# Kernel tuning notes

Measured on AMD Instinct MI355X. Metric: run time of the kernel, lower is better.

Reference implementation:

```python
import jax, jax.numpy as jnp
import numpy as np

N_NODES = 10000
N_EDGES = 160000
DIM_IN = 32
DIM_OUT = 64
DIM_EDGE_HIDDEN = 128
BOND_FDIM = 13


def setup_inputs() -> dict:
    key = jax.random.key(0)
    ks = jax.random.split(key, 10)
    s = 0.1
    x = jax.random.normal(ks[0], (N_NODES, DIM_IN), dtype=jnp.float32)
    edge_index = jax.random.randint(ks[1], (2, N_EDGES), 0, N_NODES, dtype=jnp.int64)
    edge_attr = jax.random.uniform(ks[2], (N_EDGES, BOND_FDIM), dtype=jnp.float32)
    # edge-MLP params: BOND_FDIM -> hidden -> in*out
    W1 = jax.random.normal(ks[3], (BOND_FDIM, DIM_EDGE_HIDDEN), dtype=jnp.float32) * s
    b1 = jnp.zeros((DIM_EDGE_HIDDEN,), dtype=jnp.float32)
    W2 = jax.random.normal(ks[4], (DIM_EDGE_HIDDEN, DIM_IN * DIM_OUT), dtype=jnp.float32) * s
    b2 = jnp.zeros((DIM_IN * DIM_OUT,), dtype=jnp.float32)
    # NNConv root weight + bias
    root = jax.random.normal(ks[5], (DIM_IN, DIM_OUT), dtype=jnp.float32) * s
    bias = jnp.zeros((DIM_OUT,), dtype=jnp.float32)
    return {"x": x, "edge_index": edge_index, "edge_attr": edge_attr,
            "W1": W1, "b1": b1, "W2": W2, "b2": b2, "root": root, "bias": bias}


def reference(x, edge_index, edge_attr, W1, b1, W2, b2, root, bias):
    src, dst = edge_index[0], edge_index[1]  # PyG: row=source j, col=target i
    # edge MLP -> per-edge weight matrix [E, in, out]
    h = jax.nn.relu(edge_attr @ W1 + b1)
    w = (h @ W2 + b2).reshape(-1, DIM_IN, DIM_OUT)
    # gather source features, per-edge matmul -> messages [E, out]
    msg = jnp.einsum('ei,eio->eo', x[src], w)
    # scatter-add to target nodes
    agg = jax.ops.segment_sum(msg, dst, num_segments=N_NODES)
    out = agg + x @ root + bias
    return jax.nn.relu(out)
```

## Files before the change

kernel.cpp:

```cpp
#include <hip/hip_runtime.h>

#define N_NODES 10000
#define N_EDGES 160000
#define DIM_IN 32
#define DIM_OUT 64
#define DIM_HID 128
#define BOND 13
#define NB 4
#define NGROUPS (N_NODES / NB)
#define CAP 96

typedef _Float16 half2_t __attribute__((ext_vector_type(2)));
typedef _Float16 f16x8 __attribute__((ext_vector_type(8)));
typedef float f32x4 __attribute__((ext_vector_type(4)));
typedef unsigned int uint;
typedef unsigned short ushort;

static __device__ __forceinline__ float fdot2u(uint a, uint b, float c) {
#if __has_builtin(__builtin_amdgcn_fdot2)
    return __builtin_amdgcn_fdot2(__builtin_bit_cast(half2_t, a),
                                  __builtin_bit_cast(half2_t, b), c, false);
#else
    half2_t ha = __builtin_bit_cast(half2_t, a);
    half2_t hb = __builtin_bit_cast(half2_t, b);
    return c + (float)ha.x * (float)hb.x + (float)ha.y * (float)hb.y;
#endif
}

static __device__ __forceinline__ uint packh2(float a, float b) {
    half2_t h;
    h.x = (_Float16)a; h.y = (_Float16)b;
    return __builtin_bit_cast(uint, h);
}

static __device__ __forceinline__ int swz(int o, int kp) { return (o + kp) & 63; }

struct EScr {
    int      eids[64];
    int      dsts[64];
    _Float16 ea16[16][32];
    _Float16 hbuf16[16][136];
};

__global__ void prep_kernel(const float* __restrict__ W2, uint* __restrict__ W2p,
                            const float* __restrict__ W1, uint4* __restrict__ W1p,
                            const int* __restrict__ ei, int* __restrict__ cnt,
                            int* __restrict__ es,
                            const float* __restrict__ x, const float* __restrict__ root,
                            const float* __restrict__ bias, float* __restrict__ out) {
    int idx = blockIdx.x * 256 + threadIdx.x;
    if (idx < 16 * 64 * DIM_HID) {
        int ip = idx >> 13;
        int o  = (idx >> 7) & 63;
        int k  = idx & 127;
        float lo = W2[k * 2048 + (2 * ip) * 64 + o];
        float hi = W2[k * 2048 + (2 * ip + 1) * 64 + o];
        W2p[idx] = packh2(lo, hi);
    }
    if (idx < 512) {
        int nh = idx >> 6, lane = idx & 63;
        int quad = lane >> 4, l15 = lane & 15;
        int col = nh * 16 + l15;
        uint u[4];
#pragma unroll
        for (int jp = 0; jp < 4; ++jp) {
            int k0 = quad * 8 + 2 * jp, k1 = k0 + 1;
            float f0 = (k0 < BOND) ? W1[k0 * DIM_HID + col] : 0.f;
            float f1 = (k1 < BOND) ? W1[k1 * DIM_HID + col] : 0.f;
            u[jp] = packh2(f0, f1);
        }
        W1p[idx] = make_uint4(u[0], u[1], u[2], u[3]);
    }
    if (idx < N_NODES * DIM_OUT) {
        int n = idx >> 6, o = idx & 63;
        float r = bias[o];
        const float* xn = x + n * DIM_IN;
#pragma unroll 8
        for (int i = 0; i < DIM_IN; ++i) r += xn[i] * root[i * DIM_OUT + o];
        out[idx] = r;
    }
    if (idx < N_EDGES) {
        int src = ei[idx];
        int slot = atomicAdd(&cnt[src], 1);
        if (slot < CAP) es[src * CAP + slot] = idx;
    }
}

__global__ __launch_bounds__(256) void phase1_kernel(
    const float* __restrict__ x, const int* __restrict__ ei,
    const float* __restrict__ ea, const uint4* __restrict__ W1p,
    const float* __restrict__ b1, const uint* __restrict__ W2p,
    const float* __restrict__ b2, const int* __restrict__ cnt,
    const int* __restrict__ es, float* __restrict__ out)
{
    __shared__ uint  Ph[NB][DIM_HID / 2][DIM_OUT];
    __shared__ float xs_t[DIM_IN][NB];
    __shared__ uint  xsp[DIM_IN / 2][NB];

    const int t  = threadIdx.x;
    const int o  = t & 63;
    const int w  = t >> 6;
    const int n0 = blockIdx.x * NB;
    const int l15  = o & 15;
    const int quad = o >> 4;

    if (t < DIM_IN * NB) {
        int i = t >> 2, j = t & 3;
        xs_t[i][j] = x[(n0 + j) * DIM_IN + i];
    }
    __syncthreads();
    if (t < (DIM_IN / 2) * NB) {
        int ip = t >> 2, j = t & 3;
        xsp[ip][j] = packh2(xs_t[2 * ip][j], xs_t[2 * ip + 1][j]);
    }
    __syncthreads();

#pragma unroll 1
    for (int ot = 0; ot < 4; ++ot) {
        float acc[2][NB][4];
#pragma unroll
        for (int l = 0; l < 2; ++l)
#pragma unroll
            for (int j = 0; j < NB; ++j)
#pragma unroll
                for (int q = 0; q < 4; ++q) acc[l][j][q] = 0.f;
#pragma unroll 4
        for (int ip = 0; ip < 16; ++ip) {
            const uint4* base4 = (const uint4*)W2p + ((ip * 64 + ot * 16) << 5);
            uint4 wv0 = base4[w * 128 + o];
            uint4 wv1 = base4[w * 128 + 64 + o];
            uint xp0 = xsp[ip][0], xp1 = xsp[ip][1];
            uint xp2 = xsp[ip][2], xp3 = xsp[ip][3];
#define ACC4(l, wv, xp, j) \
            acc[l][j][0] = fdot2u(xp, wv.x, acc[l][j][0]); \
            acc[l][j][1] = fdot2u(xp, wv.y, acc[l][j][1]); \
            acc[l][j][2] = fdot2u(xp, wv.z, acc[l][j][2]); \
            acc[l][j][3] = fdot2u(xp, wv.w, acc[l][j][3]);
            ACC4(0, wv0, xp0, 0) ACC4(0, wv0, xp1, 1)
            ACC4(0, wv0, xp2, 2) ACC4(0, wv0, xp3, 3)
            ACC4(1, wv1, xp0, 0) ACC4(1, wv1, xp1, 1)
            ACC4(1, wv1, xp2, 2) ACC4(1, wv1, xp3, 3)
#undef ACC4
        }
        const int lhi = o >> 5;
        const int kq  = o & 31;
        const int o0 = ot * 16 + w * 4 + lhi;
        const int o1 = o0 + 2;
        const int kp0 = 2 * kq, kp1 = 2 * kq + 1;
#pragma unroll
        for (int j = 0; j < NB; ++j) {
            Ph[j][kp0][swz(o0, kp0)] = packh2(acc[0][j][0], acc[0][j][1]);
            Ph[j][kp1][swz(o0, kp1)] = packh2(acc[0][j][2], acc[0][j][3]);
            Ph[j][kp0][swz(o1, kp0)] = packh2(acc[1][j][0], acc[1][j][1]);
            Ph[j][kp1][swz(o1, kp1)] = packh2(acc[1][j][2], acc[1][j][3]);
        }
    }
    __syncthreads();

    f16x8 pregf[16];
#pragma unroll
    for (int nt = 0; nt < 4; ++nt)
#pragma unroll
        for (int kk = 0; kk < 4; ++kk) {
            const int col = nt * 16 + l15;
            uint4 u;
            int kp = kk * 16 + quad * 4;
            u.x = Ph[w][kp + 0][swz(col, kp + 0)];
            u.y = Ph[w][kp + 1][swz(col, kp + 1)];
            u.z = Ph[w][kp + 2][swz(col, kp + 2)];
            u.w = Ph[w][kp + 3][swz(col, kp + 3)];
            pregf[nt * 4 + kk] = __builtin_bit_cast(f16x8, u);
        }

    float qv[4] = {0.f, 0.f, 0.f, 0.f};
#pragma unroll 4
    for (int i = 0; i < DIM_IN; ++i) {
        float xv = xs_t[i][w];
#pragma unroll
        for (int nt = 0; nt < 4; ++nt)
            qv[nt] += xv * b2[i * DIM_OUT + nt * 16 + l15];
    }

    f16x8 w1f[8];
    float b1v[8];
#pragma unroll
    for (int nh = 0; nh < 8; ++nh) {
        w1f[nh] = __builtin_bit_cast(f16x8, W1p[nh * 64 + o]);
        b1v[nh] = b1[nh * 16 + l15];
    }

    EScr* S = (EScr*)&Ph[w][0][0];
    const int n = n0 + w;
    const int start = n * CAP;
    int deg = cnt[n];
    deg = deg < CAP ? deg : CAP;

    __builtin_amdgcn_wave_barrier();
    ((uint4*)S->ea16)[o] = make_uint4(0u, 0u, 0u, 0u);
    __builtin_amdgcn_wave_barrier();

#pragma unroll 1
    for (int gbase = 0; gbase < deg; gbase += 64) {
        const int cnt64 = (deg - gbase < 64) ? (deg - gbase) : 64;
        __builtin_amdgcn_wave_barrier();
        if (o < cnt64) {
            int e = es[start + gbase + o];
            S->eids[o] = e;
            S->dsts[o] = ei[N_EDGES + e];
        }
        __builtin_amdgcn_wave_barrier();
        const int ntiles = (cnt64 + 15) >> 4;
#pragma unroll 1
        for (int tb = 0; tb < ntiles; ++tb) {
            const int tilebase = tb * 16;
            const int tcnt = (cnt64 - tilebase < 16) ? (cnt64 - tilebase) : 16;
            __builtin_amdgcn_wave_barrier();
            if (l15 < BOND) {
#pragma unroll
                for (int r = 0; r < 4; ++r) {
                    int p = quad + 4 * r;
                    if (p < tcnt) {
                        float v = ea[(long)S->eids[tilebase + p] * BOND + l15];
                        S->ea16[p][l15] = (_Float16)v;
                    }
                }
            }
            __builtin_amdgcn_wave_barrier();
            const f16x8 af = *(const f16x8*)&S->ea16[l15][quad * 8];
#pragma unroll
            for (int nh = 0; nh < 8; ++nh) {
                f32x4 hacc = {0.f, 0.f, 0.f, 0.f};
                hacc = __builtin_amdgcn_mfma_f32_16x16x32_f16(af, w1f[nh], hacc, 0, 0, 0);
#pragma unroll
                for (int r = 0; r < 4; ++r) {
                    float hv = hacc[r] + b1v[nh];
                    S->hbuf16[quad * 4 + r][nh * 16 + l15] =
                        (_Float16)(hv > 0.f ? hv : 0.f);
                }
            }
            __builtin_amdgcn_wave_barrier();
            f16x8 hf[4];
#pragma unroll
            for (int kk = 0; kk < 4; ++kk)
                hf[kk] = *(const f16x8*)&S->hbuf16[l15][kk * 32 + quad * 8];
            int dstv[4];
#pragma unroll
            for (int r = 0; r < 4; ++r)
                dstv[r] = S->dsts[tilebase + quad * 4 + r];
#pragma unroll
            for (int nt = 0; nt < 4; ++nt) {
                f32x4 acc = {0.f, 0.f, 0.f, 0.f};
#pragma unroll
                for (int kk = 0; kk < 4; ++kk)
                    acc = __builtin_amdgcn_mfma_f32_16x16x32_f16(
                              hf[kk], pregf[nt * 4 + kk], acc, 0, 0, 0);
#pragma unroll
                for (int r = 0; r < 4; ++r) {
                    if (quad * 4 + r < tcnt)
                        atomicAdd(&out[(long)dstv[r] * DIM_OUT + nt * 16 + l15],
                                  acc[r] + qv[nt]);
                }
            }
        }
    }
}

__global__ __launch_bounds__(256) void relu_kernel(float* __restrict__ out) {
    int idx = blockIdx.x * 256 + threadIdx.x;
    if (idx < N_NODES * DIM_OUT) {
        float v = out[idx];
        out[idx] = v > 0.f ? v : 0.f;
    }
}


extern "C" void kernel_launch(void* const* d_in, const int* in_sizes, int n_in,
                              void* d_out, int out_size, void* d_ws, size_t ws_size,
                              hipStream_t stream) {
    const float* x    = (const float*)d_in[0];
    const int*   ei   = (const int*)d_in[1];
    const float* ea   = (const float*)d_in[2];
    const float* W1   = (const float*)d_in[3];
    const float* b1   = (const float*)d_in[4];
    const float* W2   = (const float*)d_in[5];
    const float* b2   = (const float*)d_in[6];
    const float* root = (const float*)d_in[7];
    const float* bias = (const float*)d_in[8];
    float* out = (float*)d_out;
    char* ws = (char*)d_ws;

    int*   cnt = (int*)(ws + 0);
    int*   es  = (int*)(ws + 40064);
    uint*  W2p = (uint*)(ws + 3880064);
    uint4* W1p = (uint4*)(ws + 4404352);

    hipMemsetAsync(cnt, 0, 40064, stream);
    prep_kernel<<<2500, 256, 0, stream>>>(W2, W2p, W1, W1p, ei, cnt, es,
                                          x, root, bias, out);
    phase1_kernel<<<NGROUPS, 256, 0, stream>>>(x, ei, ea, W1p, b1, W2p, b2,
                                               cnt, es, out);
    relu_kernel<<<2500, 256, 0, stream>>>(out);
}
```

Baseline: 199.1 us.

## Compute per-node projected W2 with MFMA and split node edges across two waves

```diff
diff --git a/kernel.cpp b/kernel.cpp
--- a/kernel.cpp
+++ b/kernel.cpp
@@ -6,7 +6,7 @@
 #define DIM_OUT 64
 #define DIM_HID 128
 #define BOND 13
-#define NB 4
+#define NB 8
 #define NGROUPS (N_NODES / NB)
 #define CAP 96
 
@@ -14,18 +14,6 @@
 typedef _Float16 f16x8 __attribute__((ext_vector_type(8)));
 typedef float f32x4 __attribute__((ext_vector_type(4)));
 typedef unsigned int uint;
-typedef unsigned short ushort;
-
-static __device__ __forceinline__ float fdot2u(uint a, uint b, float c) {
-#if __has_builtin(__builtin_amdgcn_fdot2)
-    return __builtin_amdgcn_fdot2(__builtin_bit_cast(half2_t, a),
-                                  __builtin_bit_cast(half2_t, b), c, false);
-#else
-    half2_t ha = __builtin_bit_cast(half2_t, a);
-    half2_t hb = __builtin_bit_cast(half2_t, b);
-    return c + (float)ha.x * (float)hb.x + (float)ha.y * (float)hb.y;
-#endif
-}
 
 static __device__ __forceinline__ uint packh2(float a, float b) {
     half2_t h;
@@ -36,26 +24,29 @@
 static __device__ __forceinline__ int swz(int o, int kp) { return (o + kp) & 63; }
 
 struct EScr {
-    int      eids[64];
-    int      dsts[64];
+    int      eids[16];
+    int      dsts[16];
     _Float16 ea16[16][32];
     _Float16 hbuf16[16][136];
 };
 
-__global__ void prep_kernel(const float* __restrict__ W2, uint* __restrict__ W2p,
+__global__ void prep_kernel(const float* __restrict__ W2, uint4* __restrict__ W2p,
                             const float* __restrict__ W1, uint4* __restrict__ W1p,
                             const int* __restrict__ ei, int* __restrict__ cnt,
                             int* __restrict__ es,
                             const float* __restrict__ x, const float* __restrict__ root,
                             const float* __restrict__ bias, float* __restrict__ out) {
     int idx = blockIdx.x * 256 + threadIdx.x;
-    if (idx < 16 * 64 * DIM_HID) {
-        int ip = idx >> 13;
-        int o  = (idx >> 7) & 63;
-        int k  = idx & 127;
-        float lo = W2[k * 2048 + (2 * ip) * 64 + o];
-        float hi = W2[k * 2048 + (2 * ip + 1) * 64 + o];
-        W2p[idx] = packh2(lo, hi);
+    if (idx < 512 * 64) {
+        int f = idx >> 6, lane = idx & 63;
+        int k = f >> 2, of = f & 3;
+        int q = lane >> 4, l15 = lane & 15;
+        const float* base = W2 + k * 2048 + q * 512 + of * 16 + l15;
+        uint u0 = packh2(base[0],   base[64]);
+        uint u1 = packh2(base[128], base[192]);
+        uint u2 = packh2(base[256], base[320]);
+        uint u3 = packh2(base[384], base[448]);
+        W2p[idx] = make_uint4(u0, u1, u2, u3);
     }
     if (idx < 512) {
         int nh = idx >> 6, lane = idx & 63;
@@ -86,16 +77,14 @@
     }
 }
 
-__global__ __launch_bounds__(256) void phase1_kernel(
+__global__ __launch_bounds__(1024, 4) void phase1_kernel(
     const float* __restrict__ x, const int* __restrict__ ei,
     const float* __restrict__ ea, const uint4* __restrict__ W1p,
-    const float* __restrict__ b1, const uint* __restrict__ W2p,
+    const float* __restrict__ b1, const uint4* __restrict__ W2p,
     const float* __restrict__ b2, const int* __restrict__ cnt,
     const int* __restrict__ es, float* __restrict__ out)
 {
     __shared__ uint  Ph[NB][DIM_HID / 2][DIM_OUT];
-    __shared__ float xs_t[DIM_IN][NB];
-    __shared__ uint  xsp[DIM_IN / 2][NB];
 
     const int t  = threadIdx.x;
     const int o  = t & 63;
@@ -104,59 +93,50 @@
     const int l15  = o & 15;
     const int quad = o >> 4;
 
-    if (t < DIM_IN * NB) {
-        int i = t >> 2, j = t & 3;
-        xs_t[i][j] = x[(n0 + j) * DIM_IN + i];
+    f16x8 af;
+    {
+        uint ua[4];
+        const float* xn8 = x + (long)(n0 + l15) * DIM_IN;
+#pragma unroll
+        for (int jj = 0; jj < 4; ++jj) {
+            float a0 = 0.f, a1 = 0.f;
+            if (l15 < NB) {
+                a0 = xn8[quad * 8 + 2 * jj];
+                a1 = xn8[quad * 8 + 2 * jj + 1];
+            }
+            ua[jj] = packh2(a0, a1);
+        }
+        af = __builtin_bit_cast(f16x8, make_uint4(ua[0], ua[1], ua[2], ua[3]));
+    }
+
+    {
+        const int of = w & 3;
+        const int kbase = (w >> 2) * 32;
+        const int oo = of * 16 + l15;
+#pragma unroll 2
+        for (int m = 0; m < 16; ++m) {
+            const int k0 = kbase + 2 * m;
+            const uint4 bu0 = W2p[(k0 * 4 + of) * 64 + o];
+            const uint4 bu1 = W2p[((k0 + 1) * 4 + of) * 64 + o];
+            f32x4 D0 = {0.f, 0.f, 0.f, 0.f};
+            f32x4 D1 = {0.f, 0.f, 0.f, 0.f};
+            D0 = __builtin_amdgcn_mfma_f32_16x16x32_f16(
+                     af, __builtin_bit_cast(f16x8, bu0), D0, 0, 0, 0);
+            D1 = __builtin_amdgcn_mfma_f32_16x16x32_f16(
+                     af, __builtin_bit_cast(f16x8, bu1), D1, 0, 0, 0);
+            if (o < 32) {
+                const int kp = (kbase >> 1) + m;
+                const int sc = swz(oo, kp);
+#pragma unroll
+                for (int r = 0; r < 4; ++r)
+                    Ph[quad * 4 + r][kp][sc] = packh2(D0[r], D1[r]);
+            }
+        }
     }
     __syncthreads();
-    if (t < (DIM_IN / 2) * NB) {
-        int ip = t >> 2, j = t & 3;
-        xsp[ip][j] = packh2(xs_t[2 * ip][j], xs_t[2 * ip + 1][j]);
-    }
-    __syncthreads();
-
-#pragma unroll 1
-    for (int ot = 0; ot < 4; ++ot) {
-        float acc[2][NB][4];
-#pragma unroll
-        for (int l = 0; l < 2; ++l)
-#pragma unroll
-            for (int j = 0; j < NB; ++j)
-#pragma unroll
-                for (int q = 0; q < 4; ++q) acc[l][j][q] = 0.f;
-#pragma unroll 4
-        for (int ip = 0; ip < 16; ++ip) {
-            const uint4* base4 = (const uint4*)W2p + ((ip * 64 + ot * 16) << 5);
-            uint4 wv0 = base4[w * 128 + o];
-            uint4 wv1 = base4[w * 128 + 64 + o];
-            uint xp0 = xsp[ip][0], xp1 = xsp[ip][1];
-            uint xp2 = xsp[ip][2], xp3 = xsp[ip][3];
-#define ACC4(l, wv, xp, j) \
-            acc[l][j][0] = fdot2u(xp, wv.x, acc[l][j][0]); \
-            acc[l][j][1] = fdot2u(xp, wv.y, acc[l][j][1]); \
-            acc[l][j][2] = fdot2u(xp, wv.z, acc[l][j][2]); \
-            acc[l][j][3] = fdot2u(xp, wv.w, acc[l][j][3]);
-            ACC4(0, wv0, xp0, 0) ACC4(0, wv0, xp1, 1)
-            ACC4(0, wv0, xp2, 2) ACC4(0, wv0, xp3, 3)
-            ACC4(1, wv1, xp0, 0) ACC4(1, wv1, xp1, 1)
-            ACC4(1, wv1, xp2, 2) ACC4(1, wv1, xp3, 3)
-#undef ACC4
-        }
-        const int lhi = o >> 5;
-        const int kq  = o & 31;
-        const int o0 = ot * 16 + w * 4 + lhi;
-        const int o1 = o0 + 2;
-        const int kp0 = 2 * kq, kp1 = 2 * kq + 1;
-#pragma unroll
-        for (int j = 0; j < NB; ++j) {
-            Ph[j][kp0][swz(o0, kp0)] = packh2(acc[0][j][0], acc[0][j][1]);
-            Ph[j][kp1][swz(o0, kp1)] = packh2(acc[0][j][2], acc[0][j][3]);
-            Ph[j][kp0][swz(o1, kp0)] = packh2(acc[1][j][0], acc[1][j][1]);
-            Ph[j][kp1][swz(o1, kp1)] = packh2(acc[1][j][2], acc[1][j][3]);
-        }
-    }
-    __syncthreads();
-
+
+    const int nd  = w >> 1;
+    const int sub = w & 1;
     f16x8 pregf[16];
 #pragma unroll
     for (int nt = 0; nt < 4; ++nt)
@@ -165,20 +145,25 @@
             const int col = nt * 16 + l15;
             uint4 u;
             int kp = kk * 16 + quad * 4;
-            u.x = Ph[w][kp + 0][swz(col, kp + 0)];
-            u.y = Ph[w][kp + 1][swz(col, kp + 1)];
-            u.z = Ph[w][kp + 2][swz(col, kp + 2)];
-            u.w = Ph[w][kp + 3][swz(col, kp + 3)];
+            u.x = Ph[nd][kp + 0][swz(col, kp + 0)];
+            u.y = Ph[nd][kp + 1][swz(col, kp + 1)];
+            u.z = Ph[nd][kp + 2][swz(col, kp + 2)];
+            u.w = Ph[nd][kp + 3][swz(col, kp + 3)];
             pregf[nt * 4 + kk] = __builtin_bit_cast(f16x8, u);
         }
 
+    const int n = n0 + nd;
+
     float qv[4] = {0.f, 0.f, 0.f, 0.f};
+    {
+        const float* xn = x + (long)n * DIM_IN;
 #pragma unroll 4
-    for (int i = 0; i < DIM_IN; ++i) {
-        float xv = xs_t[i][w];
-#pragma unroll
-        for (int nt = 0; nt < 4; ++nt)
-            qv[nt] += xv * b2[i * DIM_OUT + nt * 16 + l15];
+        for (int i = 0; i < DIM_IN; ++i) {
+            float xv = xn[i];
+#pragma unroll
+            for (int nt = 0; nt < 4; ++nt)
+                qv[nt] += xv * b2[i * DIM_OUT + nt * 16 + l15];
+        }
     }
 
     f16x8 w1f[8];
@@ -189,77 +174,73 @@
         b1v[nh] = b1[nh * 16 + l15];
     }
 
-    EScr* S = (EScr*)&Ph[w][0][0];
-    const int n = n0 + w;
     const int start = n * CAP;
     int deg = cnt[n];
     deg = deg < CAP ? deg : CAP;
 
-    __builtin_amdgcn_wave_barrier();
+    __syncthreads();
+
+    EScr* S = (EScr*)((char*)&Ph[nd][0][0] + sub * 8192);
+
     ((uint4*)S->ea16)[o] = make_uint4(0u, 0u, 0u, 0u);
     __builtin_amdgcn_wave_barrier();
 
+    const int ntiles = (deg + 15) >> 4;
 #pragma unroll 1
-    for (int gbase = 0; gbase < deg; gbase += 64) {
-        const int cnt64 = (deg - gbase < 64) ? (deg - gbase) : 64;
-        __builtin_amdgcn_wave_barrier();
-        if (o < cnt64) {
-            int e = es[start + gbase + o];
+    for (int tb = sub; tb < ntiles; tb += 2) {
+        const int tilebase = tb * 16;
+        const int tcnt = (deg - tilebase < 16) ? (deg - tilebase) : 16;
+        __builtin_amdgcn_wave_barrier();
+        if (o < tcnt) {
+            int e = es[start + tilebase + o];
             S->eids[o] = e;
             S->dsts[o] = ei[N_EDGES + e];
         }
         __builtin_amdgcn_wave_barrier();
-        const int ntiles = (cnt64 + 15) >> 4;
-#pragma unroll 1
-        for (int tb = 0; tb < ntiles; ++tb) {
-            const int tilebase = tb * 16;
-            const int tcnt = (cnt64 - tilebase < 16) ? (cnt64 - tilebase) : 16;
-            __builtin_amdgcn_wave_barrier();
-            if (l15 < BOND) {
-#pragma unroll
-                for (int r = 0; r < 4; ++r) {
-                    int p = quad + 4 * r;
-                    if (p < tcnt) {
-                        float v = ea[(long)S->eids[tilebase + p] * BOND + l15];
-                        S->ea16[p][l15] = (_Float16)v;
-                    }
+        if (l15 < BOND) {
+#pragma unroll
+            for (int r = 0; r < 4; ++r) {
+                int p = quad + 4 * r;
+                if (p < tcnt) {
+                    float v = ea[(long)S->eids[p] * BOND + l15];
+                    S->ea16[p][l15] = (_Float16)v;
                 }
             }
-            __builtin_amdgcn_wave_barrier();
-            const f16x8 af = *(const f16x8*)&S->ea16[l15][quad * 8];
-#pragma unroll
-            for (int nh = 0; nh < 8; ++nh) {
-                f32x4 hacc = {0.f, 0.f, 0.f, 0.f};
-                hacc = __builtin_amdgcn_mfma_f32_16x16x32_f16(af, w1f[nh], hacc, 0, 0, 0);
-#pragma unroll
-                for (int r = 0; r < 4; ++r) {
-                    float hv = hacc[r] + b1v[nh];
-                    S->hbuf16[quad * 4 + r][nh * 16 + l15] =
-                        (_Float16)(hv > 0.f ? hv : 0.f);
-                }
-            }
-            __builtin_amdgcn_wave_barrier();
-            f16x8 hf[4];
+        }
+        __builtin_amdgcn_wave_barrier();
+        const f16x8 aef = *(const f16x8*)&S->ea16[l15][quad * 8];
+#pragma unroll
+        for (int nh = 0; nh < 8; ++nh) {
+            f32x4 hacc = {0.f, 0.f, 0.f, 0.f};
+            hacc = __builtin_amdgcn_mfma_f32_16x16x32_f16(aef, w1f[nh], hacc, 0, 0, 0);
+#pragma unroll
+            for (int r = 0; r < 4; ++r) {
+                float hv = hacc[r] + b1v[nh];
+                S->hbuf16[quad * 4 + r][nh * 16 + l15] =
+                    (_Float16)(hv > 0.f ? hv : 0.f);
+            }
+        }
+        __builtin_amdgcn_wave_barrier();
+        f16x8 hf[4];
+#pragma unroll
+        for (int kk = 0; kk < 4; ++kk)
+            hf[kk] = *(const f16x8*)&S->hbuf16[l15][kk * 32 + quad * 8];
+        int dstv[4];
+#pragma unroll
+        for (int r = 0; r < 4; ++r)
+            dstv[r] = S->dsts[quad * 4 + r];
+#pragma unroll
+        for (int nt = 0; nt < 4; ++nt) {
+            f32x4 acc = {0.f, 0.f, 0.f, 0.f};
 #pragma unroll
             for (int kk = 0; kk < 4; ++kk)
-                hf[kk] = *(const f16x8*)&S->hbuf16[l15][kk * 32 + quad * 8];
-            int dstv[4];
-#pragma unroll
-            for (int r = 0; r < 4; ++r)
-                dstv[r] = S->dsts[tilebase + quad * 4 + r];
-#pragma unroll
-            for (int nt = 0; nt < 4; ++nt) {
-                f32x4 acc = {0.f, 0.f, 0.f, 0.f};
-#pragma unroll
-                for (int kk = 0; kk < 4; ++kk)
-                    acc = __builtin_amdgcn_mfma_f32_16x16x32_f16(
-                              hf[kk], pregf[nt * 4 + kk], acc, 0, 0, 0);
-#pragma unroll
-                for (int r = 0; r < 4; ++r) {
-                    if (quad * 4 + r < tcnt)
-                        atomicAdd(&out[(long)dstv[r] * DIM_OUT + nt * 16 + l15],
-                                  acc[r] + qv[nt]);
-                }
+                acc = __builtin_amdgcn_mfma_f32_16x16x32_f16(
+                          hf[kk], pregf[nt * 4 + kk], acc, 0, 0, 0);
+#pragma unroll
+            for (int r = 0; r < 4; ++r) {
+                if (quad * 4 + r < tcnt)
+                    atomicAdd(&out[(long)dstv[r] * DIM_OUT + nt * 16 + l15],
+                              acc[r] + qv[nt]);
             }
         }
     }
@@ -291,13 +272,13 @@
 
     int*   cnt = (int*)(ws + 0);
     int*   es  = (int*)(ws + 40064);
-    uint*  W2p = (uint*)(ws + 3880064);
+    uint4* W2p = (uint4*)(ws + 3880064);
     uint4* W1p = (uint4*)(ws + 4404352);
 
     hipMemsetAsync(cnt, 0, 40064, stream);
     prep_kernel<<<2500, 256, 0, stream>>>(W2, W2p, W1, W1p, ei, cnt, es,
                                           x, root, bias, out);
-    phase1_kernel<<<NGROUPS, 256, 0, stream>>>(x, ei, ea, W1p, b1, W2p, b2,
-                                               cnt, es, out);
+    phase1_kernel<<<NGROUPS, 1024, 0, stream>>>(x, ei, ea, W1p, b1, W2p, b2,
+                                                cnt, es, out);
     relu_kernel<<<2500, 256, 0, stream>>>(out);
 }
```

New measurement: 243.8 us. 1.22x slower.
